# Kernel tuning notes

Hardware: AMD Instinct MI355X
Metric: run time of the kernel (lower is better)

Reference implementation:

```python
import jax, jax.numpy as jnp
import numpy as np

N = 512      # nodes
E = 16384    # edges (avg degree 32)
D = 128      # indim
OUT = 128    # outdim


def setup_inputs() -> dict:
    key = jax.random.key(0)
    k1, k2, k3 = jax.random.split(key, 3)
    X = jax.random.normal(k1, (N, N, D), dtype=jnp.float32)
    edge_index = jax.random.randint(k2, (2, E), 0, N, dtype=jnp.int64)
    W = jax.random.normal(k3, (3 * D, OUT), dtype=jnp.float32) * (1.0 / np.sqrt(3 * D))
    b = jnp.zeros((OUT,), dtype=jnp.float32)
    return {"X": X, "edge_index": edge_index, "W": W, "b": b}


def reference(X, edge_index, W, b):
    # X: [N, N, D] tuple features X[i, j] for (subgraph root i, node j)
    # edge_index: [2, E] directed edges (src -> dst), aggr = 'sum'
    n = X.shape[0]
    src, dst = edge_index[0], edge_index[1]
    # Dense binary adjacency (sum aggregation counts multi-edges, matching
    # scatter-add over the edge list). A[k, j] = #edges k -> j.
    A = jnp.zeros((n, n), dtype=X.dtype).at[src, dst].add(jnp.ones((src.shape[0],), X.dtype))
    # OpMessagePassingOnSubg2D: within subgraph i, aggregate over neighbors of j
    # X1[i, j] = sum_{k in N(j)} X[i, k]
    X1 = jnp.einsum('kj,ikd->ijd', A, X)
    # OpMessagePassingCrossSubg2D: across subgraphs, aggregate over neighbors of i
    # X2[i, j] = sum_{k in N(i)} X[k, j]
    X2 = jnp.einsum('ki,kjd->ijd', A, X)
    # catvalue([X1, X2]) -> [X, X1, X2], then pointwise MLP (single Linear)
    H = jnp.concatenate([X, X1, X2], axis=-1)  # [N, N, 3D]
    return H @ W + b  # [N, N, OUT]
```

## Files before the change

kernel.cpp:

```cpp
#include <hip/hip_runtime.h>
#include <hip/hip_bf16.h>

#define NN 512
#define DD 128
#define EE 16384
#define K3 384

typedef __attribute__((ext_vector_type(8))) short bf16x8;
typedef __attribute__((ext_vector_type(4))) short bf16x4;
typedef __attribute__((ext_vector_type(4))) float f32x4;

__device__ inline short f2bf(float f) {
    union { __hip_bfloat16 h; short s; } u;
    u.h = __float2bfloat16(f);
    return u.s;
}


__global__ void k_zero(float* __restrict__ At) {
    At[blockIdx.x * 256 + threadIdx.x] = 0.0f;
}

__global__ void k_edges(const int* __restrict__ ei, float* __restrict__ At) {
    __shared__ int flag;
    if (threadIdx.x == 0) flag = 0;
    __syncthreads();
    int any = 0;
    for (int i = threadIdx.x; i < EE; i += blockDim.x) any |= ei[2 * i + 1];
    if (any) atomicOr(&flag, 1);
    __syncthreads();
    const bool is32 = (flag != 0);
    for (int e = threadIdx.x; e < EE; e += blockDim.x) {
        int src, dst;
        if (is32) { src = ei[e];     dst = ei[EE + e]; }
        else      { src = ei[2 * e]; dst = ei[2 * (EE + e)]; }
        atomicAdd(&At[dst * NN + src], 1.0f);
    }
}

__global__ void k_wt(const float* __restrict__ W, short* __restrict__ Wt) {
    int t = blockIdx.x * 256 + threadIdx.x;
    int kk = t >> 7, n = t & 127;
    Wt[n * K3 + kk] = f2bf(W[t]);
}

__global__ __launch_bounds__(256) void k_agg(const float* __restrict__ X,
                                             const float* __restrict__ At,
                                             short* __restrict__ X1b,
                                             short* __restrict__ X2b) {
    __shared__ short As[128 * 72];
    __shared__ short Bs[128 * 72];

    const int tid  = threadIdx.x;
    const int lane = tid & 63;
    const int wv   = tid >> 6;
    const int wr   = (wv >> 1) * 64;
    const int wc   = (wv & 1) * 64;
    const int lm   = lane & 15;
    const int lq   = lane >> 4;

    int a0, Bbase, Bks, Cbase, Crs;
    short* Cp;
    const int bidx = blockIdx.x;
    if (bidx < 2048) {
        int i = bidx >> 2, jt = bidx & 3;
        a0 = jt * 128; Bbase = i * 65536; Bks = 128;
        Cbase = i * 65536 + jt * 16384; Crs = 128; Cp = X1b;
    } else {
        int bb = bidx - 2048;
        int j = bb >> 2, it = bb & 3;
        a0 = it * 128; Bbase = j * 128; Bks = 65536;
        Cbase = it * 8388608 + j * 128; Crs = 65536; Cp = X2b;
    }

    f32x4 acc[4][4] = {};

    const int d  = tid & 127;
    const int kh = tid >> 7;

    for (int kb = 0; kb < 8; ++kb) {
        const int k0 = kb * 64;
        #pragma unroll
        for (int it8 = 0; it8 < 8; ++it8) {
            int g = tid + it8 * 256;
            int r = g >> 4, kq = (g & 15) * 4;
            float4 v = *(const float4*)&At[(a0 + r) * 512 + k0 + kq];
            bf16x4 p; p[0] = f2bf(v.x); p[1] = f2bf(v.y); p[2] = f2bf(v.z); p[3] = f2bf(v.w);
            *(bf16x4*)&As[r * 72 + kq] = p;
        }
        #pragma unroll
        for (int gi = 0; gi < 4; ++gi) {
            int kg = kh * 4 + gi;
            bf16x8 p;
            #pragma unroll
            for (int j = 0; j < 8; ++j)
                p[j] = f2bf(X[Bbase + (k0 + kg * 8 + j) * Bks + d]);
            *(bf16x8*)&Bs[d * 72 + kg * 8] = p;
        }
        __syncthreads();
        #pragma unroll
        for (int ks = 0; ks < 2; ++ks) {
            bf16x8 af[4], bfr[4];
            #pragma unroll
            for (int mf = 0; mf < 4; ++mf)
                af[mf] = *(const bf16x8*)&As[(wr + mf * 16 + lm) * 72 + ks * 32 + lq * 8];
            #pragma unroll
            for (int nf = 0; nf < 4; ++nf)
                bfr[nf] = *(const bf16x8*)&Bs[(wc + nf * 16 + lm) * 72 + ks * 32 + lq * 8];
            #pragma unroll
            for (int mf = 0; mf < 4; ++mf)
                #pragma unroll
                for (int nf = 0; nf < 4; ++nf)
                    acc[mf][nf] = __builtin_amdgcn_mfma_f32_16x16x32_bf16(
                        af[mf], bfr[nf], acc[mf][nf], 0, 0, 0);
        }
        __syncthreads();
    }

    #pragma unroll
    for (int mf = 0; mf < 4; ++mf)
        #pragma unroll
        for (int nf = 0; nf < 4; ++nf)
            #pragma unroll
            for (int r = 0; r < 4; ++r) {
                int row = wr + mf * 16 + lq * 4 + r;
                int col = wc + nf * 16 + lm;
                Cp[Cbase + row * Crs + col] = f2bf(acc[mf][nf][r]);
            }
}

__global__ __launch_bounds__(256) void k_final(const float* __restrict__ X,
                                               const short* __restrict__ X1b,
                                               const short* __restrict__ X2b,
                                               const short* __restrict__ Wt,
                                               const float* __restrict__ bias,
                                               float* __restrict__ out) {
    __shared__ short As[128 * 72];
    __shared__ short Ws[128 * 72];

    const int tid  = threadIdx.x;
    const int lane = tid & 63;
    const int wv   = tid >> 6;
    const int wr   = (wv >> 1) * 64;
    const int wc   = (wv & 1) * 64;
    const int lm   = lane & 15;
    const int lq   = lane >> 4;
    const int m0   = blockIdx.x * 128;

    f32x4 acc[4][4] = {};

    for (int ph = 0; ph < 6; ++ph) {
        const int s = ph >> 1, h = ph & 1;
        if (s == 0) {
            #pragma unroll
            for (int it8 = 0; it8 < 8; ++it8) {
                int g = tid + it8 * 256;
                int r = g >> 4, kq = (g & 15) * 4;
                float4 v = *(const float4*)&X[(m0 + r) * 128 + h * 64 + kq];
                bf16x4 p; p[0] = f2bf(v.x); p[1] = f2bf(v.y); p[2] = f2bf(v.z); p[3] = f2bf(v.w);
                *(bf16x4*)&As[r * 72 + kq] = p;
            }
        } else {
            const short* src = (s == 1) ? X1b : X2b;
            #pragma unroll
            for (int it4 = 0; it4 < 4; ++it4) {
                int g = tid + it4 * 256;
                int r = g >> 3, ko = (g & 7) * 8;
                *(bf16x8*)&As[r * 72 + ko] =
                    *(const bf16x8*)&src[(m0 + r) * 128 + h * 64 + ko];
            }
        }
        #pragma unroll
        for (int it4 = 0; it4 < 4; ++it4) {
            int g = tid + it4 * 256;
            int n = g >> 3, ko = (g & 7) * 8;
            *(bf16x8*)&Ws[n * 72 + ko] =
                *(const bf16x8*)&Wt[n * K3 + s * 128 + h * 64 + ko];
        }
        __syncthreads();
        #pragma unroll
        for (int ks = 0; ks < 2; ++ks) {
            bf16x8 af[4], bfr[4];
            #pragma unroll
            for (int mf = 0; mf < 4; ++mf)
                af[mf] = *(const bf16x8*)&As[(wr + mf * 16 + lm) * 72 + ks * 32 + lq * 8];
            #pragma unroll
            for (int nf = 0; nf < 4; ++nf)
                bfr[nf] = *(const bf16x8*)&Ws[(wc + nf * 16 + lm) * 72 + ks * 32 + lq * 8];
            #pragma unroll
            for (int mf = 0; mf < 4; ++mf)
                #pragma unroll
                for (int nf = 0; nf < 4; ++nf)
                    acc[mf][nf] = __builtin_amdgcn_mfma_f32_16x16x32_bf16(
                        af[mf], bfr[nf], acc[mf][nf], 0, 0, 0);
        }
        __syncthreads();
    }

    #pragma unroll
    for (int nf = 0; nf < 4; ++nf) {
        float bv = bias[wc + nf * 16 + lm];
        #pragma unroll
        for (int mf = 0; mf < 4; ++mf)
            #pragma unroll
            for (int r = 0; r < 4; ++r) {
                int row = m0 + wr + mf * 16 + lq * 4 + r;
                int col = wc + nf * 16 + lm;
                out[row * 128 + col] = acc[mf][nf][r] + bv;
            }
    }
}

extern "C" void kernel_launch(void* const* d_in, const int* in_sizes, int n_in,
                              void* d_out, int out_size, void* d_ws, size_t ws_size,
                              hipStream_t stream) {
    const float* X  = (const float*)d_in[0];
    const int*   ei = (const int*)d_in[1];
    const float* W  = (const float*)d_in[2];
    const float* b  = (const float*)d_in[3];
    float* out = (float*)d_out;

    float* At  = (float*)d_ws;
    short* Wt  = (short*)((char*)d_ws + (size_t)(1u << 20));
    short* X1b = (short*)((char*)d_ws + (size_t)(2u << 20));
    short* X2b = (short*)((char*)d_ws + (size_t)(2u << 20) + (size_t)(64u << 20));

    k_zero <<<1024, 256, 0, stream>>>(At);
    k_edges<<<1, 1024, 0, stream>>>(ei, At);
    k_wt   <<<192, 256, 0, stream>>>(W, Wt);
    k_agg  <<<4096, 256, 0, stream>>>(X, At, X1b, X2b);
    k_final<<<2048, 256, 0, stream>>>(X, X1b, X2b, Wt, b, out);
}
```

Baseline: 502.9 us.

## Pre-transpose X to bf16 and use async global-to-LDS loads with swizzled tiles

Adds a prep kernel that converts X to bf16 and writes two transposed copies, so both aggregation GEMMs read K-contiguous operands. Adjacency is cast to bf16 once instead of per tile. The aggregation and final GEMMs load tiles with global_load_lds into XOR-swizzled LDS and stage output through LDS for vectorized stores. The cost is an extra full pass over X and a larger workspace; the old path is kept as a fallback when the workspace is too small.

After: 513.5 us. 2.1% more time.

```diff
diff --git a/kernel.cpp b/kernel.cpp
--- a/kernel.cpp
+++ b/kernel.cpp
@@ -1,19 +1,26 @@
 #include <hip/hip_runtime.h>
 #include <hip/hip_bf16.h>
+#include <stdint.h>
 
 #define NN 512
 #define DD 128
 #define EE 16384
 #define K3 384
 
-typedef __attribute__((ext_vector_type(8))) short bf16x8;
-typedef __attribute__((ext_vector_type(4))) short bf16x4;
-typedef __attribute__((ext_vector_type(4))) float f32x4;
-
-__device__ inline short f2bf(float f) {
+typedef short bf16x8 __attribute__((ext_vector_type(8)));
+typedef short bf16x4 __attribute__((ext_vector_type(4)));
+typedef float f32x4  __attribute__((ext_vector_type(4)));
+
+__device__ __forceinline__ short f2bf(float f) {
     union { __hip_bfloat16 h; short s; } u;
     u.h = __float2bfloat16(f);
     return u.s;
+}
+
+typedef __attribute__((address_space(3))) unsigned int lds_u32;
+typedef __attribute__((address_space(1))) const unsigned int glb_u32;
+__device__ __forceinline__ void gll16(void* l, const void* g) {
+    __builtin_amdgcn_global_load_lds((glb_u32*)g, (lds_u32*)l, 16, 0, 0);
 }
 
 
@@ -38,18 +45,66 @@
     }
 }
 
+__global__ void k_cast_at(const float* __restrict__ At, short* __restrict__ Atb) {
+    int t = blockIdx.x * 256 + threadIdx.x;
+    Atb[t] = f2bf(At[t]);
+}
+
 __global__ void k_wt(const float* __restrict__ W, short* __restrict__ Wt) {
     int t = blockIdx.x * 256 + threadIdx.x;
     int kk = t >> 7, n = t & 127;
     Wt[n * K3 + kk] = f2bf(W[t]);
 }
 
-__global__ __launch_bounds__(256) void k_agg(const float* __restrict__ X,
-                                             const float* __restrict__ At,
-                                             short* __restrict__ X1b,
-                                             short* __restrict__ X2b) {
-    __shared__ short As[128 * 72];
-    __shared__ short Bs[128 * 72];
+__global__ __launch_bounds__(256) void k_prep(const float* __restrict__ X,
+                                              short* __restrict__ XbT,
+                                              short* __restrict__ XT2) {
+    __shared__ __align__(16) short T[128 * 128];
+    const int tid = threadIdx.x;
+    const int b = blockIdx.x;
+    int sbase, rstride, dbase;
+    short* dst;
+    if (b < 2048) {
+        int i = b >> 2, k0 = (b & 3) * 128;
+        sbase = i * 65536 + k0 * 128; rstride = 128;
+        dbase = i * 65536 + k0; dst = XbT;
+    } else {
+        int bb = b - 2048;
+        int j = bb >> 2, i0 = (bb & 3) * 128;
+        sbase = i0 * 65536 + j * 128; rstride = 65536;
+        dbase = j * 65536 + i0; dst = XT2;
+    }
+    #pragma unroll
+    for (int it = 0; it < 16; ++it) {
+        int g = tid + it * 256;
+        int r = g >> 5, c4 = (g & 31) * 4;
+        float4 v = *(const float4*)&X[sbase + r * rstride + c4];
+        bf16x4 p; p[0] = f2bf(v.x); p[1] = f2bf(v.y); p[2] = f2bf(v.z); p[3] = f2bf(v.w);
+        int cs = c4 ^ (((r >> 3) & 7) << 2);
+        *(bf16x4*)&T[r * 128 + cs] = p;
+    }
+    __syncthreads();
+    #pragma unroll
+    for (int it = 0; it < 8; ++it) {
+        int q = tid + it * 256;
+        int d = q >> 4, ck = (q & 15) * 8;
+        bf16x8 p;
+        #pragma unroll
+        for (int j = 0; j < 8; ++j) {
+            int k = ck + j;
+            p[j] = T[k * 128 + (d ^ (((k >> 3) & 7) << 2))];
+        }
+        *(bf16x8*)&dst[dbase + d * 512 + ck] = p;
+    }
+}
+
+__global__ __launch_bounds__(256) void k_aggg(const short* __restrict__ Atb,
+                                              const short* __restrict__ Bsrc,
+                                              short* __restrict__ C,
+                                              int mode) {
+    __shared__ __align__(16) short sm[16384];
+    short* As = sm;
+    short* Bs = sm + 8192;
 
     const int tid  = threadIdx.x;
     const int lane = tid & 63;
@@ -59,6 +114,179 @@
     const int lm   = lane & 15;
     const int lq   = lane >> 4;
 
+    const int inst = blockIdx.x >> 2, t4 = blockIdx.x & 3;
+    const int a0 = t4 * 128;
+    const int Bbase = inst * 65536;
+    int Cbase, Crs;
+    if (mode == 0) { Cbase = inst * 65536 + t4 * 16384; Crs = 128; }
+    else           { Cbase = t4 * 8388608 + inst * 128; Crs = 65536; }
+
+    int srow[4], scg[4];
+    #pragma unroll
+    for (int it = 0; it < 4; ++it) {
+        int s = it * 256 + tid;
+        int r = s >> 3, p = s & 7;
+        srow[it] = r; scg[it] = (p ^ (r & 7)) * 8;
+    }
+
+    f32x4 acc[4][4] = {};
+
+    for (int kb = 0; kb < 8; ++kb) {
+        const int k0 = kb * 64;
+        #pragma unroll
+        for (int it = 0; it < 4; ++it) {
+            int slot = it * 256 + tid;
+            gll16(&As[slot * 8], &Atb[(a0 + srow[it]) * 512 + k0 + scg[it]]);
+            gll16(&Bs[slot * 8], &Bsrc[Bbase + srow[it] * 512 + k0 + scg[it]]);
+        }
+        __syncthreads();
+        #pragma unroll
+        for (int ks = 0; ks < 2; ++ks) {
+            bf16x8 af[4], bf[4];
+            #pragma unroll
+            for (int mf = 0; mf < 4; ++mf) {
+                int R = wr + mf * 16 + lm, Cc = ks * 4 + lq;
+                af[mf] = *(const bf16x8*)&As[R * 64 + (Cc ^ (R & 7)) * 8];
+            }
+            #pragma unroll
+            for (int nf = 0; nf < 4; ++nf) {
+                int R = wc + nf * 16 + lm, Cc = ks * 4 + lq;
+                bf[nf] = *(const bf16x8*)&Bs[R * 64 + (Cc ^ (R & 7)) * 8];
+            }
+            #pragma unroll
+            for (int mf = 0; mf < 4; ++mf)
+                #pragma unroll
+                for (int nf = 0; nf < 4; ++nf)
+                    acc[mf][nf] = __builtin_amdgcn_mfma_f32_16x16x32_bf16(
+                        af[mf], bf[nf], acc[mf][nf], 0, 0, 0);
+        }
+        __syncthreads();
+    }
+
+    #pragma unroll
+    for (int mf = 0; mf < 4; ++mf)
+        #pragma unroll
+        for (int nf = 0; nf < 4; ++nf)
+            #pragma unroll
+            for (int r = 0; r < 4; ++r)
+                sm[(wr + mf * 16 + lq * 4 + r) * 128 + wc + nf * 16 + lm]
+                    = f2bf(acc[mf][nf][r]);
+    __syncthreads();
+    #pragma unroll
+    for (int it = 0; it < 8; ++it) {
+        int q = tid + it * 256;
+        int orow = q >> 4, oc = (q & 15) * 8;
+        *(bf16x8*)&C[Cbase + orow * Crs + oc] = *(const bf16x8*)&sm[orow * 128 + oc];
+    }
+}
+
+__global__ __launch_bounds__(256) void k_final2(const float* __restrict__ X,
+                                                const short* __restrict__ X1b,
+                                                const short* __restrict__ X2b,
+                                                const short* __restrict__ Wt,
+                                                const float* __restrict__ bias,
+                                                float* __restrict__ out) {
+    __shared__ __align__(16) short sm[16384];
+    short* As = sm;
+    short* Ws = sm + 8192;
+
+    const int tid  = threadIdx.x;
+    const int lane = tid & 63;
+    const int wv   = tid >> 6;
+    const int wr   = (wv >> 1) * 64;
+    const int wc   = (wv & 1) * 64;
+    const int lm   = lane & 15;
+    const int lq   = lane >> 4;
+    const int m0   = blockIdx.x * 128;
+
+    int srow[4], scg[4];
+    #pragma unroll
+    for (int it = 0; it < 4; ++it) {
+        int s = it * 256 + tid;
+        int r = s >> 3, p = s & 7;
+        srow[it] = r; scg[it] = (p ^ (r & 7)) * 8;
+    }
+
+    f32x4 acc[4][4] = {};
+
+    for (int ph = 0; ph < 6; ++ph) {
+        const int s = ph >> 1, h = ph & 1;
+        const int kw0 = s * 128 + h * 64;
+        if (s == 0) {
+            #pragma unroll
+            for (int it = 0; it < 4; ++it) {
+                int slot = it * 256 + tid;
+                const float* xp = &X[(m0 + srow[it]) * 128 + h * 64 + scg[it]];
+                float4 v0 = *(const float4*)xp;
+                float4 v1 = *(const float4*)(xp + 4);
+                bf16x8 pk;
+                pk[0] = f2bf(v0.x); pk[1] = f2bf(v0.y); pk[2] = f2bf(v0.z); pk[3] = f2bf(v0.w);
+                pk[4] = f2bf(v1.x); pk[5] = f2bf(v1.y); pk[6] = f2bf(v1.z); pk[7] = f2bf(v1.w);
+                *(bf16x8*)&As[slot * 8] = pk;
+            }
+        } else {
+            const short* src = (s == 1) ? X1b : X2b;
+            #pragma unroll
+            for (int it = 0; it < 4; ++it)
+                gll16(&As[(it * 256 + tid) * 8],
+                      &src[(m0 + srow[it]) * 128 + h * 64 + scg[it]]);
+        }
+        #pragma unroll
+        for (int it = 0; it < 4; ++it)
+            gll16(&Ws[(it * 256 + tid) * 8],
+                  &Wt[srow[it] * K3 + kw0 + scg[it]]);
+        __syncthreads();
+        #pragma unroll
+        for (int ks = 0; ks < 2; ++ks) {
+            bf16x8 af[4], bf[4];
+            #pragma unroll
+            for (int mf = 0; mf < 4; ++mf) {
+                int R = wr + mf * 16 + lm, Cc = ks * 4 + lq;
+                af[mf] = *(const bf16x8*)&As[R * 64 + (Cc ^ (R & 7)) * 8];
+            }
+            #pragma unroll
+            for (int nf = 0; nf < 4; ++nf) {
+                int R = wc + nf * 16 + lm, Cc = ks * 4 + lq;
+                bf[nf] = *(const bf16x8*)&Ws[R * 64 + (Cc ^ (R & 7)) * 8];
+            }
+            #pragma unroll
+            for (int mf = 0; mf < 4; ++mf)
+                #pragma unroll
+                for (int nf = 0; nf < 4; ++nf)
+                    acc[mf][nf] = __builtin_amdgcn_mfma_f32_16x16x32_bf16(
+                        af[mf], bf[nf], acc[mf][nf], 0, 0, 0);
+        }
+        __syncthreads();
+    }
+
+    #pragma unroll
+    for (int nf = 0; nf < 4; ++nf) {
+        float bv = bias[wc + nf * 16 + lm];
+        #pragma unroll
+        for (int mf = 0; mf < 4; ++mf)
+            #pragma unroll
+            for (int r = 0; r < 4; ++r) {
+                int row = m0 + wr + mf * 16 + lq * 4 + r;
+                int col = wc + nf * 16 + lm;
+                out[row * 128 + col] = acc[mf][nf][r] + bv;
+            }
+    }
+}
+
+
+__global__ __launch_bounds__(256) void k_agg_fb(const float* __restrict__ X,
+                                                const float* __restrict__ At,
+                                                short* __restrict__ X1b,
+                                                short* __restrict__ X2b) {
+    __shared__ short As[128 * 72];
+    __shared__ short Bs[128 * 72];
+    const int tid  = threadIdx.x;
+    const int lane = tid & 63;
+    const int wv   = tid >> 6;
+    const int wr   = (wv >> 1) * 64;
+    const int wc   = (wv & 1) * 64;
+    const int lm   = lane & 15;
+    const int lq   = lane >> 4;
     int a0, Bbase, Bks, Cbase, Crs;
     short* Cp;
     const int bidx = blockIdx.x;
@@ -72,12 +300,9 @@
         a0 = it * 128; Bbase = j * 128; Bks = 65536;
         Cbase = it * 8388608 + j * 128; Crs = 65536; Cp = X2b;
     }
-
     f32x4 acc[4][4] = {};
-
     const int d  = tid & 127;
     const int kh = tid >> 7;
-
     for (int kb = 0; kb < 8; ++kb) {
         const int k0 = kb * 64;
         #pragma unroll
@@ -116,7 +341,6 @@
         }
         __syncthreads();
     }
-
     #pragma unroll
     for (int mf = 0; mf < 4; ++mf)
         #pragma unroll
@@ -129,15 +353,14 @@
             }
 }
 
-__global__ __launch_bounds__(256) void k_final(const float* __restrict__ X,
-                                               const short* __restrict__ X1b,
-                                               const short* __restrict__ X2b,
-                                               const short* __restrict__ Wt,
-                                               const float* __restrict__ bias,
-                                               float* __restrict__ out) {
+__global__ __launch_bounds__(256) void k_final_fb(const float* __restrict__ X,
+                                                  const short* __restrict__ X1b,
+                                                  const short* __restrict__ X2b,
+                                                  const short* __restrict__ Wt,
+                                                  const float* __restrict__ bias,
+                                                  float* __restrict__ out) {
     __shared__ short As[128 * 72];
     __shared__ short Ws[128 * 72];
-
     const int tid  = threadIdx.x;
     const int lane = tid & 63;
     const int wv   = tid >> 6;
@@ -146,9 +369,7 @@
     const int lm   = lane & 15;
     const int lq   = lane >> 4;
     const int m0   = blockIdx.x * 128;
-
     f32x4 acc[4][4] = {};
-
     for (int ph = 0; ph < 6; ++ph) {
         const int s = ph >> 1, h = ph & 1;
         if (s == 0) {
@@ -196,7 +417,6 @@
         }
         __syncthreads();
     }
-
     #pragma unroll
     for (int nf = 0; nf < 4; ++nf) {
         float bv = bias[wc + nf * 16 + lm];
@@ -219,15 +439,31 @@
     const float* W  = (const float*)d_in[2];
     const float* b  = (const float*)d_in[3];
     float* out = (float*)d_out;
-
-    float* At  = (float*)d_ws;
-    short* Wt  = (short*)((char*)d_ws + (size_t)(1u << 20));
-    short* X1b = (short*)((char*)d_ws + (size_t)(2u << 20));
-    short* X2b = (short*)((char*)d_ws + (size_t)(2u << 20) + (size_t)(64u << 20));
+    char* ws = (char*)d_ws;
+    const size_t MB = 1u << 20;
+
+    float* At  = (float*)ws;
+    short* Atb = (short*)(ws + 1 * MB);
+    short* Wt  = (short*)(ws + 1 * MB + 512 * 1024);
 
     k_zero <<<1024, 256, 0, stream>>>(At);
     k_edges<<<1, 1024, 0, stream>>>(ei, At);
     k_wt   <<<192, 256, 0, stream>>>(W, Wt);
-    k_agg  <<<4096, 256, 0, stream>>>(X, At, X1b, X2b);
-    k_final<<<2048, 256, 0, stream>>>(X, X1b, X2b, Wt, b, out);
-}
+
+    if (ws_size >= 194 * MB) {
+        short* X1b = (short*)(ws + 2 * MB);
+        short* XT2 = (short*)(ws + 66 * MB);
+        short* XbT = (short*)(ws + 130 * MB);
+        short* X2b = XbT;
+        k_cast_at<<<1024, 256, 0, stream>>>(At, Atb);
+        k_prep   <<<4096, 256, 0, stream>>>(X, XbT, XT2);
+        k_aggg   <<<2048, 256, 0, stream>>>(Atb, XbT, X1b, 0);
+        k_aggg   <<<2048, 256, 0, stream>>>(Atb, XT2, X2b, 1);
+        k_final2 <<<2048, 256, 0, stream>>>(X, X1b, X2b, Wt, b, out);
+    } else {
+        short* X1b = (short*)(ws + 2 * MB);
+        short* X2b = (short*)(ws + 66 * MB);
+        k_agg_fb  <<<4096, 256, 0, stream>>>(X, At, X1b, X2b);
+        k_final_fb<<<2048, 256, 0, stream>>>(X, X1b, X2b, Wt, b, out);
+    }
+}
```
